# Optimization experiments

Hardware: AMD Instinct MI355X
Metric: run time of the kernel (lower is better)

Reference implementation:

```python
import jax, jax.numpy as jnp
import numpy as np

INPUT_DIM = 1024
EMBED_DIM = 1024
NUM_HEADS = 16
HEAD_DIM = EMBED_DIM // NUM_HEADS


def _xavier_uniform(key, shape):
    fan_in, fan_out = shape[1], shape[0]
    limit = float(np.sqrt(6.0 / (fan_in + fan_out)))
    return jax.random.uniform(key, shape, jnp.float32, -limit, limit)


def setup_inputs() -> dict:
    key = jax.random.key(0)
    kx, kqkv, ko = jax.random.split(key, 3)
    x = jax.random.normal(kx, (2, 2048, INPUT_DIM), jnp.float32)
    # torch Linear stores weight as [out, in]; we keep that convention
    w_qkv = _xavier_uniform(kqkv, (3 * EMBED_DIM, INPUT_DIM))
    b_qkv = jnp.zeros((3 * EMBED_DIM,), jnp.float32)
    w_o = _xavier_uniform(ko, (EMBED_DIM, EMBED_DIM))
    b_o = jnp.zeros((EMBED_DIM,), jnp.float32)
    return {"x": x, "w_qkv": w_qkv, "b_qkv": b_qkv, "w_o": w_o, "b_o": b_o}


def reference(x, w_qkv, b_qkv, w_o, b_o):
    B, S, _ = x.shape
    H, D = NUM_HEADS, HEAD_DIM
    qkv = jnp.einsum("bsi,oi->bso", x, w_qkv) + b_qkv          # [B,S,3E]
    qkv = qkv.reshape(B, S, H, 3 * D).transpose(0, 2, 1, 3)    # [B,H,S,3D]
    q, k, v = jnp.split(qkv, 3, axis=-1)                        # each [B,H,S,D]
    scores = jnp.einsum("bhqd,bhkd->bhqk", q, k) / jnp.sqrt(jnp.float32(D))
    attn = jax.nn.softmax(scores, axis=-1)                      # [B,H,S,S]
    vals = jnp.einsum("bhqk,bhkd->bhqd", attn, v)               # [B,H,S,D]
    vals = vals.transpose(0, 2, 1, 3).reshape(B, S, H * D)      # [B,S,E]
    return jnp.einsum("bse,oe->bso", vals, w_o) + b_o
```

## Files before the change

### kernel.cpp

```cpp
#include <hip/hip_runtime.h>
#include <hip/hip_bf16.h>


typedef __attribute__((ext_vector_type(8))) short bf16x8;
typedef __attribute__((ext_vector_type(4))) short bf16x4;
typedef __attribute__((ext_vector_type(4))) float f32x4;

#define MFMA16(a, b, c) __builtin_amdgcn_mfma_f32_16x16x32_bf16((a), (b), (c), 0, 0, 0)

#if __has_builtin(__builtin_amdgcn_exp2f)
#define EXP2F(x) __builtin_amdgcn_exp2f(x)
#else
#define EXP2F(x) exp2f(x)
#endif

static __device__ __forceinline__ unsigned short f2bf_bits(float v) {
    __hip_bfloat16 h = __float2bfloat16(v);
    return *reinterpret_cast<unsigned short*>(&h);
}

static __device__ __forceinline__ bf16x8 cvt8(const float* p) {
    const f32x4 a = reinterpret_cast<const f32x4*>(p)[0];
    const f32x4 b = reinterpret_cast<const f32x4*>(p)[1];
    bf16x8 r;
    r[0] = (short)f2bf_bits(a[0]); r[1] = (short)f2bf_bits(a[1]);
    r[2] = (short)f2bf_bits(a[2]); r[3] = (short)f2bf_bits(a[3]);
    r[4] = (short)f2bf_bits(b[0]); r[5] = (short)f2bf_bits(b[1]);
    r[6] = (short)f2bf_bits(b[2]); r[7] = (short)f2bf_bits(b[3]);
    return r;
}

__device__ __forceinline__ bf16x8 ldg8(const __hip_bfloat16* p) {
    return *reinterpret_cast<const bf16x8*>(p);
}

__device__ __forceinline__ void load16_lds(const __hip_bfloat16* g, unsigned short* l) {
    __builtin_amdgcn_global_load_lds(
        (const __attribute__((address_space(1))) void*)g,
        (__attribute__((address_space(3))) void*)l, 16, 0, 0);
}

__global__ __launch_bounds__(256)
void cast2_f32_bf16(const float* __restrict__ x, __hip_bfloat16* __restrict__ xb,
                    const float* __restrict__ w, __hip_bfloat16* __restrict__ wb) {
    const int bid = blockIdx.x;
    const float* src = (bid < 512) ? x : w;
    __hip_bfloat16* dst = (bid < 512) ? xb : wb;
    const int rb = (bid < 512) ? bid : (bid - 512);
    const size_t base = (size_t)rb * 8192 + (size_t)threadIdx.x * 32;
#pragma unroll
    for (int i = 0; i < 4; ++i)
        *reinterpret_cast<bf16x8*>(dst + base + i * 8) = cvt8(src + base + i * 8);
}

__global__ __launch_bounds__(256)
void cast_f32_bf16(const float* __restrict__ src, __hip_bfloat16* __restrict__ dst) {
    const size_t base = ((size_t)blockIdx.x * 256 + threadIdx.x) * 32;
#pragma unroll
    for (int i = 0; i < 4; ++i)
        *reinterpret_cast<bf16x8*>(dst + base + i * 8) = cvt8(src + base + i * 8);
}

__global__ __launch_bounds__(256)
void qkv_gemm(const __hip_bfloat16* __restrict__ xb,
              const __hip_bfloat16* __restrict__ wb,
              const float* __restrict__ bqkv,
              __hip_bfloat16* __restrict__ Q,
              __hip_bfloat16* __restrict__ K,
              __hip_bfloat16* __restrict__ Vt) {
    __shared__ unsigned short As[2][128 * 32];
    __shared__ unsigned short Bs[2][128 * 32];

    const int tid  = threadIdx.x;
    const int lane = tid & 63;
    const int wv   = tid >> 6;
    const int quad = lane >> 4;
    const int l16  = lane & 15;
    const int wm   = wv >> 1;
    const int wn   = wv & 1;

    const int bid = blockIdx.x;
    const int xcd = bid & 7;
    const int r   = bid >> 3;
    const int m0  = (r / 3) * 128;
    const int n0  = (xcd * 3 + (r % 3)) * 128;

    const __hip_bfloat16* agl = xb + (size_t)(m0 + wv * 32 + (lane >> 2)) * 1024 + (lane & 3) * 8;
    const __hip_bfloat16* bgl = wb + (size_t)(n0 + wv * 32 + (lane >> 2)) * 1024 + (lane & 3) * 8;

    f32x4 zv = {0.f, 0.f, 0.f, 0.f};
    f32x4 acc[4][4];
#pragma unroll
    for (int ii = 0; ii < 4; ++ii)
#pragma unroll
        for (int jj = 0; jj < 4; ++jj) acc[ii][jj] = zv;

    load16_lds(agl, &As[0][(wv * 32) * 32]);
    load16_lds(agl + 16 * 1024, &As[0][(wv * 32 + 16) * 32]);
    load16_lds(bgl, &Bs[0][(wv * 32) * 32]);
    load16_lds(bgl + 16 * 1024, &Bs[0][(wv * 32 + 16) * 32]);
    __syncthreads();

    for (int k0 = 0; k0 < 1024; k0 += 32) {
        const int p = (k0 >> 5) & 1;
        if (k0 + 32 < 1024) {
            const int q = p ^ 1;
            load16_lds(agl + k0 + 32, &As[q][(wv * 32) * 32]);
            load16_lds(agl + 16 * 1024 + k0 + 32, &As[q][(wv * 32 + 16) * 32]);
            load16_lds(bgl + k0 + 32, &Bs[q][(wv * 32) * 32]);
            load16_lds(bgl + 16 * 1024 + k0 + 32, &Bs[q][(wv * 32 + 16) * 32]);
        }
        bf16x8 af[4], bf[4];
#pragma unroll
        for (int ii = 0; ii < 4; ++ii)
            af[ii] = *reinterpret_cast<const bf16x8*>(
                &As[p][(wm * 64 + ii * 16 + l16) * 32 + quad * 8]);
#pragma unroll
        for (int jj = 0; jj < 4; ++jj)
            bf[jj] = *reinterpret_cast<const bf16x8*>(
                &Bs[p][(wn * 64 + jj * 16 + l16) * 32 + quad * 8]);
#pragma unroll
        for (int ii = 0; ii < 4; ++ii)
#pragma unroll
            for (int jj = 0; jj < 4; ++jj)
                acc[ii][jj] = MFMA16(af[ii], bf[jj], acc[ii][jj]);
        __syncthreads();
    }

    const float QSCALE = 0.18033688011f;
    const int b  = m0 >> 11;
    const int s0 = m0 & 2047;

    const int nseg  = n0 + wn * 64;
    const int h     = nseg / 192;
    const int r2s   = nseg - h * 192;
    const int ttype = r2s >> 6;
    const int bh    = b * 16 + h;

    if (ttype == 2) {
#pragma unroll
        for (int jj = 0; jj < 4; ++jj) {
            const int d = jj * 16 + l16;
            const float bias = bqkv[nseg + d];
#pragma unroll
            for (int ii = 0; ii < 4; ++ii) {
                const int sk = s0 + wm * 64 + ii * 16 + quad * 4;
                bf16x4 pk;
#pragma unroll
                for (int i = 0; i < 4; ++i)
                    pk[i] = (short)f2bf_bits(acc[ii][jj][i] + bias);
                *reinterpret_cast<bf16x4*>(&Vt[((size_t)bh * 64 + d) * 2048 + sk]) = pk;
            }
        }
    } else {
        const float scl = (ttype == 0) ? QSCALE : 1.f;
        unsigned short* seg = (wn == 0) ? &As[0][0] : &Bs[0][0];
#pragma unroll
        for (int jj = 0; jj < 4; ++jj) {
            const int nl    = jj * 16 + l16;
            const float bias = bqkv[nseg + nl];
            const int cbase = nl >> 3;
            const int off   = nl & 7;
#pragma unroll
            for (int ii = 0; ii < 4; ++ii) {
#pragma unroll
                for (int i = 0; i < 4; ++i) {
                    const int m = wm * 64 + ii * 16 + quad * 4 + i;
                    const int c = cbase ^ (((m >> 2) & 3) << 1);
                    seg[m * 64 + c * 8 + off] =
                        f2bf_bits((acc[ii][jj][i] + bias) * scl);
                }
            }
        }
    }
    __syncthreads();

#pragma unroll
    for (int sgi = 0; sgi < 2; ++sgi) {
        const int nsg = n0 + sgi * 64;
        const int hh  = nsg / 192;
        const int rr  = nsg - hh * 192;
        const int tt  = rr >> 6;
        if (tt == 2) continue;
        __hip_bfloat16* gbase =
            ((tt == 0) ? Q : K) + ((size_t)(b * 16 + hh) * 2048 + s0) * 64;
        const unsigned short* seg = (sgi == 0) ? &As[0][0] : &Bs[0][0];
#pragma unroll
        for (int p4 = 0; p4 < 4; ++p4) {
            const int L = p4 * 256 + tid;
            const int m = L >> 3;
            const int c = (L & 7) ^ (((m >> 2) & 3) << 1);
            *reinterpret_cast<bf16x8*>(gbase + (size_t)L * 8) =
                *reinterpret_cast<const bf16x8*>(&seg[m * 64 + c * 8]);
        }
    }
}

__global__ __launch_bounds__(512, 4)
void attn_kernel(const __hip_bfloat16* __restrict__ Q,
                 const __hip_bfloat16* __restrict__ K,
                 const __hip_bfloat16* __restrict__ Vt,
                 __hip_bfloat16* __restrict__ AO) {
    __shared__ unsigned short SB[2][2][4096];
    __shared__ float LiX[4][2][64];

    const int tid  = threadIdx.x;
    const int lane = tid & 63;
    const int wv   = tid >> 6;
    const int grp  = wv >> 2;
    const int wq   = wv & 3;
    const int quad = lane >> 4;
    const int l16  = lane & 15;

    const int blk = blockIdx.x;
    const int xcd = blk & 7;
    const int sub = blk >> 3;
    const int bh  = xcd * 4 + (sub & 3);
    const int qb  = sub >> 2;
    const int q0  = qb * 128 + wq * 32;
    const int b   = bh >> 4;
    const int h   = bh & 15;
    const int key0 = grp * 1024;

    const __hip_bfloat16* Qp = Q  + (size_t)bh * 131072;
    const __hip_bfloat16* Kp = K  + (size_t)bh * 131072;
    const __hip_bfloat16* Vp = Vt + (size_t)bh * 131072;

    bf16x8 bQ[2][2];
#pragma unroll
    for (int t = 0; t < 2; ++t)
#pragma unroll
        for (int dh = 0; dh < 2; ++dh)
            bQ[t][dh] = ldg8(Qp + (size_t)(q0 + t * 16 + l16) * 64 + dh * 32 + quad * 8);

    const int keyg = (l16 >> 2) * 8 + (l16 & 3) + ((wq >> 1) << 2);
    const int kd0  = (wq & 1) * 32 + quad * 8;
    const __hip_bfloat16* ksrc = Kp + (size_t)(key0 + keyg) * 64 + kd0;
    const __hip_bfloat16* vsrc = Vp + (size_t)(wq * 16 + l16) * 2048 + key0 + quad * 8;

    const int gt = wq * 64 + lane;
    unsigned short* kd[2] = { &SB[grp][0][gt * 8],        &SB[grp][1][gt * 8] };
    unsigned short* vd[2] = { &SB[grp][0][gt * 8 + 2048], &SB[grp][1][gt * 8 + 2048] };

    f32x4 zv = {0.f, 0.f, 0.f, 0.f};
    f32x4 Of[2][4];
#pragma unroll
    for (int t = 0; t < 2; ++t)
#pragma unroll
        for (int jj = 0; jj < 4; ++jj) Of[t][jj] = zv;
    float li[2] = {0.f, 0.f};

    bf16x8 gk = ldg8(ksrc);
    bf16x8 gv = ldg8(vsrc);
    *reinterpret_cast<bf16x8*>(kd[0]) = gk;
    *reinterpret_cast<bf16x8*>(vd[0]) = gv;
    gk = ldg8(ksrc + 2048);
    gv = ldg8(vsrc + 32);
    __syncthreads();

    for (int kt = 0; kt < 32; ++kt) {
        const int p = kt & 1;
        if (kt < 31) {
            *reinterpret_cast<bf16x8*>(kd[p ^ 1]) = gk;
            *reinterpret_cast<bf16x8*>(vd[p ^ 1]) = gv;
        }
        if (kt < 30) {
            gk = ldg8(ksrc + (size_t)(kt + 2) * 2048);
            gv = ldg8(vsrc + (size_t)(kt + 2) * 32);
        }

        const unsigned short* base = &SB[grp][p][lane * 8];
        const bf16x8 aKA0 = *reinterpret_cast<const bf16x8*>(base + 0 * 512);
        const bf16x8 aKA1 = *reinterpret_cast<const bf16x8*>(base + 1 * 512);
        const bf16x8 aKB0 = *reinterpret_cast<const bf16x8*>(base + 2 * 512);
        const bf16x8 aKB1 = *reinterpret_cast<const bf16x8*>(base + 3 * 512);
        bf16x8 aV[4];
#pragma unroll
        for (int jj = 0; jj < 4; ++jj)
            aV[jj] = *reinterpret_cast<const bf16x8*>(base + (4 + jj) * 512);

        f32x4 sA[2], sB[2];
#pragma unroll
        for (int t = 0; t < 2; ++t) {
            sA[t] = zv; sB[t] = zv;
            sA[t] = MFMA16(aKA0, bQ[t][0], sA[t]);
            sA[t] = MFMA16(aKA1, bQ[t][1], sA[t]);
            sB[t] = MFMA16(aKB0, bQ[t][0], sB[t]);
            sB[t] = MFMA16(aKB1, bQ[t][1], sB[t]);
        }

#pragma unroll
        for (int t = 0; t < 2; ++t) {
            float pA[4], pB[4];
#pragma unroll
            for (int i = 0; i < 4; ++i) {
                pA[i] = EXP2F(sA[t][i]);
                pB[i] = EXP2F(sB[t][i]);
            }
            li[t] += ((pA[0] + pA[1]) + (pA[2] + pA[3]))
                   + ((pB[0] + pB[1]) + (pB[2] + pB[3]));

            bf16x8 bP;
            bP[0] = (short)f2bf_bits(pA[0]); bP[1] = (short)f2bf_bits(pA[1]);
            bP[2] = (short)f2bf_bits(pA[2]); bP[3] = (short)f2bf_bits(pA[3]);
            bP[4] = (short)f2bf_bits(pB[0]); bP[5] = (short)f2bf_bits(pB[1]);
            bP[6] = (short)f2bf_bits(pB[2]); bP[7] = (short)f2bf_bits(pB[3]);

#pragma unroll
            for (int jj = 0; jj < 4; ++jj)
                Of[t][jj] = MFMA16(aV[jj], bP, Of[t][jj]);
        }
        __syncthreads();
    }

#pragma unroll
    for (int t = 0; t < 2; ++t) {
        li[t] += __shfl_xor(li[t], 16);
        li[t] += __shfl_xor(li[t], 32);
    }

    f32x4* xf = reinterpret_cast<f32x4*>(&SB[0][0][0]);
    if (grp == 1) {
#pragma unroll
        for (int t = 0; t < 2; ++t) {
            LiX[wq][t][lane] = li[t];
#pragma unroll
            for (int jj = 0; jj < 4; ++jj)
                xf[wq * 512 + (t * 4 + jj) * 64 + lane] = Of[t][jj];
        }
    }
    __syncthreads();
    if (grp == 0) {
#pragma unroll
        for (int t = 0; t < 2; ++t) {
            const float linv = 1.f / (li[t] + LiX[wq][t][lane]);
            const int s = q0 + t * 16 + l16;
            __hip_bfloat16* aop = AO + (((size_t)b * 2048 + s) * 16 + h) * 64;
#pragma unroll
            for (int jj = 0; jj < 4; ++jj) {
                const f32x4 o2 = xf[wq * 512 + (t * 4 + jj) * 64 + lane];
                bf16x4 pk;
#pragma unroll
                for (int i = 0; i < 4; ++i)
                    pk[i] = (short)f2bf_bits((Of[t][jj][i] + o2[i]) * linv);
                *reinterpret_cast<bf16x4*>(aop + jj * 16 + quad * 4) = pk;
            }
        }
    }
}

__global__ __launch_bounds__(256)
void out_gemm(const __hip_bfloat16* __restrict__ A,
              const __hip_bfloat16* __restrict__ wob,
              const float* __restrict__ bo,
              float* __restrict__ out) {
    __shared__ unsigned short As[2][64 * 32];
    __shared__ unsigned short Bs[2][128 * 32];

    const int tid  = threadIdx.x;
    const int lane = tid & 63;
    const int wv   = tid >> 6;
    const int quad = lane >> 4;
    const int l16  = lane & 15;
    const int wm   = wv >> 1;
    const int wn   = wv & 1;

    const int bid = blockIdx.x;
    const int m0  = (bid >> 3) * 64;
    const int n0  = (bid & 7) * 128;

    const __hip_bfloat16* agl = A   + (size_t)(m0 + wv * 16 + (lane >> 2)) * 1024 + (lane & 3) * 8;
    const __hip_bfloat16* bgl = wob + (size_t)(n0 + wv * 32 + (lane >> 2)) * 1024 + (lane & 3) * 8;

    f32x4 zv = {0.f, 0.f, 0.f, 0.f};
    f32x4 acc[2][4];
#pragma unroll
    for (int ii = 0; ii < 2; ++ii)
#pragma unroll
        for (int jj = 0; jj < 4; ++jj) acc[ii][jj] = zv;

    load16_lds(agl, &As[0][(wv * 16) * 32]);
    load16_lds(bgl, &Bs[0][(wv * 32) * 32]);
    load16_lds(bgl + 16 * 1024, &Bs[0][(wv * 32 + 16) * 32]);
    __syncthreads();

    for (int k0 = 0; k0 < 1024; k0 += 32) {
        const int p = (k0 >> 5) & 1;
        if (k0 + 32 < 1024) {
            const int q = p ^ 1;
            load16_lds(agl + k0 + 32, &As[q][(wv * 16) * 32]);
            load16_lds(bgl + k0 + 32, &Bs[q][(wv * 32) * 32]);
            load16_lds(bgl + 16 * 1024 + k0 + 32, &Bs[q][(wv * 32 + 16) * 32]);
        }
        bf16x8 af[2], bf[4];
#pragma unroll
        for (int ii = 0; ii < 2; ++ii)
            af[ii] = *reinterpret_cast<const bf16x8*>(
                &As[p][(wm * 32 + ii * 16 + l16) * 32 + quad * 8]);
#pragma unroll
        for (int jj = 0; jj < 4; ++jj)
            bf[jj] = *reinterpret_cast<const bf16x8*>(
                &Bs[p][(wn * 64 + jj * 16 + l16) * 32 + quad * 8]);
#pragma unroll
        for (int ii = 0; ii < 2; ++ii)
#pragma unroll
            for (int jj = 0; jj < 4; ++jj)
                acc[ii][jj] = MFMA16(af[ii], bf[jj], acc[ii][jj]);
        __syncthreads();
    }

#pragma unroll
    for (int jj = 0; jj < 4; ++jj) {
        const int n = n0 + wn * 64 + jj * 16 + l16;
        const float bias = bo[n];
#pragma unroll
        for (int ii = 0; ii < 2; ++ii) {
#pragma unroll
            for (int i = 0; i < 4; ++i) {
                const int m = m0 + wm * 32 + ii * 16 + quad * 4 + i;
                out[(size_t)m * 1024 + n] = acc[ii][jj][i] + bias;
            }
        }
    }
}

extern "C" void kernel_launch(void* const* d_in, const int* in_sizes, int n_in,
                              void* d_out, int out_size, void* d_ws, size_t ws_size,
                              hipStream_t stream) {
    const float* x    = (const float*)d_in[0];
    const float* wqkv = (const float*)d_in[1];
    const float* bqkv = (const float*)d_in[2];
    const float* wo   = (const float*)d_in[3];
    const float* bo   = (const float*)d_in[4];
    float* out = (float*)d_out;

    __hip_bfloat16* ws = (__hip_bfloat16*)d_ws;
    __hip_bfloat16* Q   = ws;
    __hip_bfloat16* K   = ws + (size_t)4194304;
    __hip_bfloat16* Vt  = ws + (size_t)8388608;
    __hip_bfloat16* AO  = ws + (size_t)12582912;
    __hip_bfloat16* wob = Q;

    __hip_bfloat16* xb     = (__hip_bfloat16*)d_out;
    __hip_bfloat16* wqkvb  = xb + (size_t)4194304;

    cast2_f32_bf16<<<dim3(896), 256, 0, stream>>>(x, xb, wqkv, wqkvb);
    qkv_gemm<<<dim3(768), 256, 0, stream>>>(xb, wqkvb, bqkv, Q, K, Vt);
    attn_kernel<<<dim3(512), 512, 0, stream>>>(Q, K, Vt, AO);
    cast_f32_bf16<<<dim3(128), 256, 0, stream>>>(wo, wob);
    out_gemm<<<dim3(512), 256, 0, stream>>>(AO, wob, bo, out);
}
```

Before: 191.4 us.

## Split attention key range across four wave groups with 1024-thread blocks

Raises the attention kernel's block from 512 to 1024 threads so four wave groups each handle a quarter of the keys (512 instead of 1024), halving the serial key loop per wave. Partial outputs and row sums are reduced through shared memory in three sequential stages with extra barriers. It also brackets the MFMA sections with s_setprio to favour matrix issue. The cost is more LDS use, more synchronisation in the epilogue, and a launch bound of 8 waves per EU that may constrain registers.

```diff
diff --git a/kernel.cpp b/kernel.cpp
--- a/kernel.cpp
+++ b/kernel.cpp
@@ -196,13 +196,12 @@
     }
 }
 
-__global__ __launch_bounds__(512, 4)
+__global__ __launch_bounds__(1024, 8)
 void attn_kernel(const __hip_bfloat16* __restrict__ Q,
                  const __hip_bfloat16* __restrict__ K,
                  const __hip_bfloat16* __restrict__ Vt,
                  __hip_bfloat16* __restrict__ AO) {
-    __shared__ unsigned short SB[2][2][4096];
-    __shared__ float LiX[4][2][64];
+    __shared__ unsigned short SB[4][2][4096];
 
     const int tid  = threadIdx.x;
     const int lane = tid & 63;
@@ -220,7 +219,7 @@
     const int q0  = qb * 128 + wq * 32;
     const int b   = bh >> 4;
     const int h   = bh & 15;
-    const int key0 = grp * 1024;
+    const int key0 = grp * 512;
 
     const __hip_bfloat16* Qp = Q  + (size_t)bh * 131072;
     const __hip_bfloat16* Kp = K  + (size_t)bh * 131072;
@@ -258,13 +257,13 @@
     gv = ldg8(vsrc + 32);
     __syncthreads();
 
-    for (int kt = 0; kt < 32; ++kt) {
+    for (int kt = 0; kt < 16; ++kt) {
         const int p = kt & 1;
-        if (kt < 31) {
+        if (kt < 15) {
             *reinterpret_cast<bf16x8*>(kd[p ^ 1]) = gk;
             *reinterpret_cast<bf16x8*>(vd[p ^ 1]) = gv;
         }
-        if (kt < 30) {
+        if (kt < 14) {
             gk = ldg8(ksrc + (size_t)(kt + 2) * 2048);
             gv = ldg8(vsrc + (size_t)(kt + 2) * 32);
         }
@@ -280,6 +279,7 @@
             aV[jj] = *reinterpret_cast<const bf16x8*>(base + (4 + jj) * 512);
 
         f32x4 sA[2], sB[2];
+        __builtin_amdgcn_s_setprio(1);
 #pragma unroll
         for (int t = 0; t < 2; ++t) {
             sA[t] = zv; sB[t] = zv;
@@ -288,6 +288,7 @@
             sB[t] = MFMA16(aKB0, bQ[t][0], sB[t]);
             sB[t] = MFMA16(aKB1, bQ[t][1], sB[t]);
         }
+        __builtin_amdgcn_s_setprio(0);
 
 #pragma unroll
         for (int t = 0; t < 2; ++t) {
@@ -306,9 +307,11 @@
             bP[4] = (short)f2bf_bits(pB[0]); bP[5] = (short)f2bf_bits(pB[1]);
             bP[6] = (short)f2bf_bits(pB[2]); bP[7] = (short)f2bf_bits(pB[3]);
 
+            __builtin_amdgcn_s_setprio(1);
 #pragma unroll
             for (int jj = 0; jj < 4; ++jj)
                 Of[t][jj] = MFMA16(aV[jj], bP, Of[t][jj]);
+            __builtin_amdgcn_s_setprio(0);
         }
         __syncthreads();
     }
@@ -319,21 +322,62 @@
         li[t] += __shfl_xor(li[t], 32);
     }
 
-    f32x4* xf = reinterpret_cast<f32x4*>(&SB[0][0][0]);
+    f32x4* xf  = reinterpret_cast<f32x4*>(&SB[0][0][0]);
+    float* lix = reinterpret_cast<float*>(&SB[2][0][0]);
+
+    if (grp != 0) {
+#pragma unroll
+        for (int t = 0; t < 2; ++t)
+            lix[((grp - 1) * 4 + wq) * 128 + t * 64 + lane] = li[t];
+    }
     if (grp == 1) {
 #pragma unroll
+        for (int t = 0; t < 2; ++t)
+#pragma unroll
+            for (int jj = 0; jj < 4; ++jj)
+                xf[wq * 512 + (t * 4 + jj) * 64 + lane] = Of[t][jj];
+    }
+    __syncthreads();
+    if (grp == 0) {
+#pragma unroll
         for (int t = 0; t < 2; ++t) {
-            LiX[wq][t][lane] = li[t];
+            li[t] += lix[(0 * 4 + wq) * 128 + t * 64 + lane]
+                   + lix[(1 * 4 + wq) * 128 + t * 64 + lane]
+                   + lix[(2 * 4 + wq) * 128 + t * 64 + lane];
+#pragma unroll
+            for (int jj = 0; jj < 4; ++jj)
+                Of[t][jj] += xf[wq * 512 + (t * 4 + jj) * 64 + lane];
+        }
+    }
+    __syncthreads();
+    if (grp == 2) {
+#pragma unroll
+        for (int t = 0; t < 2; ++t)
 #pragma unroll
             for (int jj = 0; jj < 4; ++jj)
                 xf[wq * 512 + (t * 4 + jj) * 64 + lane] = Of[t][jj];
-        }
     }
     __syncthreads();
     if (grp == 0) {
 #pragma unroll
+        for (int t = 0; t < 2; ++t)
+#pragma unroll
+            for (int jj = 0; jj < 4; ++jj)
+                Of[t][jj] += xf[wq * 512 + (t * 4 + jj) * 64 + lane];
+    }
+    __syncthreads();
+    if (grp == 3) {
+#pragma unroll
+        for (int t = 0; t < 2; ++t)
+#pragma unroll
+            for (int jj = 0; jj < 4; ++jj)
+                xf[wq * 512 + (t * 4 + jj) * 64 + lane] = Of[t][jj];
+    }
+    __syncthreads();
+    if (grp == 0) {
+#pragma unroll
         for (int t = 0; t < 2; ++t) {
-            const float linv = 1.f / (li[t] + LiX[wq][t][lane]);
+            const float linv = 1.f / li[t];
             const int s = q0 + t * 16 + l16;
             __hip_bfloat16* aop = AO + (((size_t)b * 2048 + s) * 16 + h) * 64;
 #pragma unroll
@@ -446,7 +490,7 @@
 
     cast2_f32_bf16<<<dim3(896), 256, 0, stream>>>(x, xb, wqkv, wqkvb);
     qkv_gemm<<<dim3(768), 256, 0, stream>>>(xb, wqkvb, bqkv, Q, K, Vt);
-    attn_kernel<<<dim3(512), 512, 0, stream>>>(Q, K, Vt, AO);
+    attn_kernel<<<dim3(512), 1024, 0, stream>>>(Q, K, Vt, AO);
     cast_f32_bf16<<<dim3(128), 256, 0, stream>>>(wo, wob);
     out_gemm<<<dim3(512), 256, 0, stream>>>(AO, wob, bo, out);
 }
```

Result: slower. 573.0 us (+199.4%).
